# Kernel tuning notes

Measured on AMD Instinct MI355X. Metric: run time of the kernel, lower is better.

Reference implementation:

```python
import jax, jax.numpy as jnp
import numpy as np

NUM_ACTIONS = 16  # number of unique leaf actions (= output_dim)


def setup_inputs() -> dict:
    key = jax.random.key(0)
    ks = jax.random.split(key, 7)
    B, IN, D, A = 32768, 128, 511, 512
    L = D + A + 1  # 1024 leaves
    x = jax.random.normal(ks[0], (B, IN), dtype=jnp.float32)
    Wd = jax.random.normal(ks[1], (D, IN), dtype=jnp.float32) * 0.05
    bd = jax.random.normal(ks[2], (D,), dtype=jnp.float32) * 0.05
    Wa = jax.random.normal(ks[3], (A, IN), dtype=jnp.float32) * 0.05
    ba = jax.random.normal(ks[4], (A,), dtype=jnp.float32) * 0.05
    Wl = jax.random.normal(ks[5], (L, 2 * (D + A)), dtype=jnp.float32) * 0.05
    seg_ids = jax.random.randint(ks[6], (L,), 0, NUM_ACTIONS, dtype=jnp.int32)
    return {"x": x, "Wd": Wd, "bd": bd, "Wa": Wa, "ba": ba, "Wl": Wl,
            "seg_ids": seg_ids}


def reference(x, Wd, bd, Wa, ba, Wl, seg_ids):
    # dual linear heads (torch Linear: y = x @ W.T + b)
    x1 = x @ Wd.T + bd            # [B, D]
    x2 = x @ Wa.T + ba            # [B, A]
    h = jnp.concatenate([x1, x2], axis=1)                     # [B, D+A]
    hh = jnp.concatenate([jax.nn.relu(h), jax.nn.relu(-h)], axis=1)  # [B, 2(D+A)]
    leaf = hh @ Wl.T              # [B, L]
    # ragged per-action max over leaf columns (MaxPoolLayer)
    pooled = jax.ops.segment_max(leaf.T, seg_ids,
                                 num_segments=NUM_ACTIONS).T   # [B, NUM_ACTIONS]
    return jax.nn.softmax(pooled, axis=-1)
```

## Files before the change

kernel.cpp:

```cpp
#include <hip/hip_runtime.h>
#include <hip/hip_bf16.h>
#include <cstdint>
#include <cmath>

#define AS1 __attribute__((address_space(1)))
#define AS3 __attribute__((address_space(3)))

typedef unsigned short u16;
typedef uint32_t u32;
typedef __attribute__((ext_vector_type(8))) __bf16 bf16x8;
typedef __attribute__((ext_vector_type(8))) unsigned short u16x8;
typedef __attribute__((ext_vector_type(4))) float f32x4;


__device__ __forceinline__ u16 f2bf(float f) {
    uint32_t u = __builtin_bit_cast(uint32_t, f);
    return (u16)((u + 0x7fffu + ((u >> 16) & 1u)) >> 16);
}

__device__ __forceinline__ u32 f2ord(float f) {
    u32 u = __builtin_bit_cast(u32, f);
    return u ^ (u32)(((int32_t)u >> 31) | 0x80000000);
}
__device__ __forceinline__ float ord2f(u32 v) {
    u32 u = (v & 0x80000000u) ? (v ^ 0x80000000u) : ~v;
    return __builtin_bit_cast(float, u);
}


__global__ void setup_all(const float* __restrict__ x,
                          const float* __restrict__ Wd, const float* __restrict__ bd,
                          const float* __restrict__ Wa, const float* __restrict__ ba,
                          const float* __restrict__ Wl,
                          u16* __restrict__ xb, u16* __restrict__ w1b,
                          float* __restrict__ bb, u16* __restrict__ w1t,
                          u16* __restrict__ wsb, u16* __restrict__ dlb,
                          float* __restrict__ cl, u32* __restrict__ pooled) {
    __shared__ float cred[256];
    const int b = blockIdx.x;
    const int tid = threadIdx.x;
    if (b < 2048) {
        long idx = (long)(b * 256 + tid) * 8;
        float4 a = *(const float4*)(x + idx);
        float4 c = *(const float4*)(x + idx + 4);
        u16x8 o;
        o[0]=f2bf(a.x); o[1]=f2bf(a.y); o[2]=f2bf(a.z); o[3]=f2bf(a.w);
        o[4]=f2bf(c.x); o[5]=f2bf(c.y); o[6]=f2bf(c.z); o[7]=f2bf(c.w);
        *(u16x8*)(xb + idx) = o;
    } else if (b < 2112) {
        int t = (b - 2048) * 256 + tid;
        int row = t >> 4, g = (t & 15) * 8;
        const float* src = nullptr;
        if (row < 511)       src = Wd + row * 128 + g;
        else if (row < 1023) src = Wa + (row - 511) * 128 + g;
        u16x8 o = 0;
        if (src) {
            #pragma unroll
            for (int j = 0; j < 8; ++j) o[j] = f2bf(src[j]);
        }
        *(u16x8*)(w1b + row * 128 + g) = o;
        #pragma unroll
        for (int j = 0; j < 8; ++j) w1t[(g + j) * 1024 + row] = o[j];
        if ((t & 15) == 0)
            bb[row] = row < 511 ? bd[row] : (row < 1023 ? ba[row - 511] : 0.f);
    } else if (b < 2624) {
        const int l0 = (b - 2112) * 2;
        const int lo = tid >> 7, g = (tid & 127) * 8;
        const float* src = Wl + (long)(l0 + lo) * 2046;
        u16x8 os, od;
        float part = 0.f;
        #pragma unroll
        for (int j = 0; j < 8; ++j) {
            int c = g + j;
            float pa = 0.f, pb = 0.f;
            if (c < 1023) { pa = src[c]; pb = src[1023 + c]; }
            os[j] = f2bf(0.5f * (pa + pb));
            float v = pa - pb;
            od[j] = f2bf(v);
            float b1 = c < 511 ? bd[c] : (c < 1023 ? ba[c - 511] : 0.f);
            part += v * b1;
        }
        *(u16x8*)(wsb + (long)(l0 + lo) * 1024 + g) = os;
        *(u16x8*)(dlb + (long)(l0 + lo) * 1024 + g) = od;
        cred[tid] = part;
        __syncthreads();
        if (tid < 2) {
            float s = 0.f;
            #pragma unroll
            for (int k = 0; k < 128; ++k) s += cred[tid * 128 + k];
            cl[l0 + tid] = 0.5f * s;
        }
    } else {
        uint4* p4 = (uint4*)pooled;
        const int base = (b - 2624) * 16384;
        #pragma unroll
        for (int j = 0; j < 64; ++j)
            p4[base + tid + j * 256] = uint4{0u, 0u, 0u, 0u};
    }
}

__global__ __launch_bounds__(256) void gemm_hwc(
        const u16* __restrict__ xb, const u16* __restrict__ w1b,
        const float* __restrict__ bb,
        const u16* __restrict__ dlb, const u16* __restrict__ w1t,
        u16* __restrict__ habs, u16* __restrict__ wcb) {
    __shared__ union SharedU {
        struct { u16 As[2][4096]; u16 Bs[2][4096]; } s;
        u16 obuf[128 * 132];
    } sh;
    const int tid  = threadIdx.x;
    const int lane = tid & 63, wave = tid >> 6;
    const int wy = wave >> 1, wx = wave & 1;
    const int i16 = lane & 15, q = lane >> 4;
    const int cA = wave * 2, srow = lane >> 2;
    const int scol = (((lane & 3) ^ ((lane >> 3) & 3))) * 8;
    const int qa   = (q ^ ((i16 >> 1) & 3)) * 8;

    f32x4 acc[4][4];
    #pragma unroll
    for (int m = 0; m < 4; ++m)
        #pragma unroll
        for (int n = 0; n < 4; ++n) acc[m][n] = f32x4{0.f,0.f,0.f,0.f};

    if (blockIdx.y == 0) {
        const long blockM = (long)blockIdx.x * 128;
        const int koff = (blockIdx.x * 4) & 31;
        const u16* a0 = dlb + (blockM + cA * 16 + srow) * 1024 + scol;
        const u16* a1 = dlb + (blockM + (cA + 1) * 16 + srow) * 1024 + scol;
        const u16* b0 = w1t + (long)(cA * 16 + srow) * 1024 + scol;
        const u16* b1 = w1t + (long)((cA + 1) * 16 + srow) * 1024 + scol;
        for (int it = 0; it < 32; ++it) {
            const int k0 = ((it + koff) & 31) << 5;
            __builtin_amdgcn_global_load_lds((const AS1 void*)(a0 + k0), (AS3 void*)&sh.s.As[0][cA * 512],       16, 0, 0);
            __builtin_amdgcn_global_load_lds((const AS1 void*)(a1 + k0), (AS3 void*)&sh.s.As[0][(cA + 1) * 512], 16, 0, 0);
            __builtin_amdgcn_global_load_lds((const AS1 void*)(b0 + k0), (AS3 void*)&sh.s.Bs[0][cA * 512],       16, 0, 0);
            __builtin_amdgcn_global_load_lds((const AS1 void*)(b1 + k0), (AS3 void*)&sh.s.Bs[0][(cA + 1) * 512], 16, 0, 0);
            __syncthreads();
            bf16x8 af[4], bfv[4];
            #pragma unroll
            for (int s = 0; s < 4; ++s) {
                af[s]  = *(const bf16x8*)&sh.s.As[0][(wy * 64 + s * 16 + i16) * 32 + qa];
                bfv[s] = *(const bf16x8*)&sh.s.Bs[0][(wx * 64 + s * 16 + i16) * 32 + qa];
            }
            #pragma unroll
            for (int sm = 0; sm < 4; ++sm)
                #pragma unroll
                for (int sn = 0; sn < 4; ++sn)
                    acc[sm][sn] = __builtin_amdgcn_mfma_f32_16x16x32_bf16(af[sm], bfv[sn], acc[sm][sn], 0, 0, 0);
            __syncthreads();
        }
        #pragma unroll
        for (int sm = 0; sm < 4; ++sm)
            #pragma unroll
            for (int sn = 0; sn < 4; ++sn) {
                const int col = wx * 64 + sn * 16 + i16;
                #pragma unroll
                for (int r = 0; r < 4; ++r) {
                    const long row = blockM + wy * 64 + sm * 16 + 4 * q + r;
                    wcb[row * 128 + col] = f2bf(0.5f * acc[sm][sn][r]);
                }
            }
        return;
    }

    const int xcd = blockIdx.x, yy = blockIdx.y - 1;
    const long blockM = (long)(xcd * 32 + (yy >> 3)) * 128;
    const int  blockN = (yy & 7) * 128;
    const int  koff = (yy >> 3) & 1;

    const u16* a0 = xb + (blockM + cA * 16 + srow) * 128 + scol;
    const u16* a1 = xb + (blockM + (cA + 1) * 16 + srow) * 128 + scol;
    const u16* b0 = w1b + ((long)blockN + cA * 16 + srow) * 128 + scol;
    const u16* b1 = w1b + ((long)blockN + (cA + 1) * 16 + srow) * 128 + scol;
    for (int it = 0; it < 2; ++it) {
        const int k0 = ((it + koff) & 1) << 6;
        #pragma unroll
        for (int p = 0; p < 2; ++p) {
            const int kp = k0 + p * 32;
            __builtin_amdgcn_global_load_lds((const AS1 void*)(a0 + kp), (AS3 void*)&sh.s.As[p][cA * 512],       16, 0, 0);
            __builtin_amdgcn_global_load_lds((const AS1 void*)(a1 + kp), (AS3 void*)&sh.s.As[p][(cA + 1) * 512], 16, 0, 0);
            __builtin_amdgcn_global_load_lds((const AS1 void*)(b0 + kp), (AS3 void*)&sh.s.Bs[p][cA * 512],       16, 0, 0);
            __builtin_amdgcn_global_load_lds((const AS1 void*)(b1 + kp), (AS3 void*)&sh.s.Bs[p][(cA + 1) * 512], 16, 0, 0);
        }
        __syncthreads();
        #pragma unroll
        for (int p = 0; p < 2; ++p) {
            bf16x8 af[4], bfv[4];
            #pragma unroll
            for (int s = 0; s < 4; ++s) {
                af[s]  = *(const bf16x8*)&sh.s.As[p][(wy * 64 + s * 16 + i16) * 32 + qa];
                bfv[s] = *(const bf16x8*)&sh.s.Bs[p][(wx * 64 + s * 16 + i16) * 32 + qa];
            }
            #pragma unroll
            for (int sm = 0; sm < 4; ++sm)
                #pragma unroll
                for (int sn = 0; sn < 4; ++sn)
                    acc[sm][sn] = __builtin_amdgcn_mfma_f32_16x16x32_bf16(af[sm], bfv[sn], acc[sm][sn], 0, 0, 0);
        }
        __syncthreads();
    }

    float bv[4];
    #pragma unroll
    for (int sn = 0; sn < 4; ++sn) bv[sn] = bb[blockN + wx * 64 + sn * 16 + i16];
    #pragma unroll
    for (int sm = 0; sm < 4; ++sm)
        #pragma unroll
        for (int sn = 0; sn < 4; ++sn)
            #pragma unroll
            for (int r = 0; r < 4; ++r)
                sh.obuf[(wy * 64 + sm * 16 + 4 * q + r) * 132 + wx * 64 + sn * 16 + i16] =
                    f2bf(fabsf(acc[sm][sn][r] + bv[sn]));
    __syncthreads();
    const int cg = (tid & 15) * 8;
    #pragma unroll
    for (int it = 0; it < 8; ++it) {
        const int row = it * 16 + (tid >> 4);
        *(u16x8*)&habs[(blockM + row) * 1024 + blockN + cg] =
            *(const u16x8*)&sh.obuf[row * 132 + cg];
    }
}

__global__ __launch_bounds__(512, 2) void gemm_leaf(const u16* __restrict__ habs,
        const u16* __restrict__ xb, const u16* __restrict__ wsb,
        const u16* __restrict__ wcb, const float* __restrict__ cl,
        const int* __restrict__ seg, u32* __restrict__ pooled) {
    __shared__ __align__(16) u16 As[4][256 * 32];
    __shared__ __align__(16) u16 Bs[4][256 * 32];
    __shared__ u32 pmax[256 * 16];
    const int tid  = threadIdx.x;
    const int lane = tid & 63, w = tid >> 6;
    const int wm = w >> 2, wn = w & 3;
    const int i16 = lane & 15, q = lane >> 4;

    const int bid  = blockIdx.x;
    const int wgid = (bid & 7) * 64 + (bid >> 3);
    const int mT = wgid >> 2, nT = wgid & 3;
    const long blockM = (long)mT * 256;
    const int  blockN = nT * 256;

    #pragma unroll
    for (int j = 0; j < 8; ++j) pmax[tid + j * 512] = 0u;

    const int r0 = tid >> 2;
    const int scol = (((tid & 3) ^ ((tid >> 3) & 3))) * 8;
    const u16* gA1 = habs + (blockM + r0) * 1024 + scol;
    const u16* gB1 = wsb  + (long)(blockN + r0) * 1024 + scol;
    const u16* gA2 = xb   + (blockM + r0) * 128 + scol;
    const u16* gB2 = wcb  + (long)(blockN + r0) * 128 + scol;
    const int ldsb = w * 512;

    auto stageA = [&](int tt) {
        u16* dst = &As[tt & 3][ldsb];
        const u16* g; int jstr;
        if (tt < 32) { g = gA1 + tt * 32;        jstr = 128 * 1024; }
        else         { g = gA2 + (tt - 32) * 32; jstr = 128 * 128; }
        __builtin_amdgcn_global_load_lds((const AS1 void*)g,          (AS3 void*)dst,          16, 0, 0);
        __builtin_amdgcn_global_load_lds((const AS1 void*)(g + jstr), (AS3 void*)(dst + 4096), 16, 0, 0);
    };
    auto stageB = [&](int tt) {
        u16* dst = &Bs[tt & 3][ldsb];
        const u16* g; int jstr;
        if (tt < 32) { g = gB1 + tt * 32;        jstr = 128 * 1024; }
        else         { g = gB2 + (tt - 32) * 32; jstr = 128 * 128; }
        __builtin_amdgcn_global_load_lds((const AS1 void*)g,          (AS3 void*)dst,          16, 0, 0);
        __builtin_amdgcn_global_load_lds((const AS1 void*)(g + jstr), (AS3 void*)(dst + 4096), 16, 0, 0);
    };

    f32x4 acc[8][4];
    #pragma unroll
    for (int m = 0; m < 8; ++m)
        #pragma unroll
        for (int n = 0; n < 4; ++n) acc[m][n] = f32x4{0.f,0.f,0.f,0.f};
    bf16x8 a0r[4], a1r[4], br[4];

    const int rdc = (q ^ ((i16 >> 1) & 3)) * 8;
    auto lda = [&](bf16x8* ar, int slot, int mh) {
        #pragma unroll
        for (int mf = 0; mf < 4; ++mf)
            ar[mf] = *(const bf16x8*)&As[slot][(wm * 128 + mh * 64 + mf * 16 + i16) * 32 + rdc];
    };
    auto ldb = [&](int slot) {
        #pragma unroll
        for (int nf = 0; nf < 4; ++nf)
            br[nf] = *(const bf16x8*)&Bs[slot][(wn * 64 + nf * 16 + i16) * 32 + rdc];
    };
    auto mf16 = [&](const bf16x8* ar, int mh) {
        #pragma unroll
        for (int mf = 0; mf < 4; ++mf)
            #pragma unroll
            for (int nf = 0; nf < 4; ++nf)
                acc[mh * 4 + mf][nf] = __builtin_amdgcn_mfma_f32_16x16x32_bf16(
                    ar[mf], br[nf], acc[mh * 4 + mf][nf], 0, 0, 0);
    };

    stageA(0); stageB(0); stageA(1); stageB(1);
    asm volatile("s_waitcnt vmcnt(4)" ::: "memory");
    __builtin_amdgcn_s_barrier();
    __builtin_amdgcn_sched_barrier(0);
    lda(a0r, 0, 0); ldb(0);

    for (int t = 0; t < 36; ++t) {
        const int slot = t & 3;
        lda(a1r, slot, 1);
        if (t + 2 < 36) { stageA(t + 2); stageB(t + 2); }
        asm volatile("s_waitcnt lgkmcnt(4)" ::: "memory");
        __builtin_amdgcn_sched_barrier(0);
        __builtin_amdgcn_s_setprio(1);
        mf16(a0r, 0);
        __builtin_amdgcn_s_setprio(0);
        asm volatile("s_waitcnt lgkmcnt(0)" ::: "memory");
        __builtin_amdgcn_sched_barrier(0);
        __builtin_amdgcn_s_setprio(1);
        mf16(a1r, 1);
        __builtin_amdgcn_s_setprio(0);
        if (t < 34)       { asm volatile("s_waitcnt vmcnt(4)" ::: "memory"); }
        else if (t == 34) { asm volatile("s_waitcnt vmcnt(0)" ::: "memory"); }
        __builtin_amdgcn_s_barrier();
        __builtin_amdgcn_sched_barrier(0);
        if (t + 1 < 36) { lda(a0r, (t + 1) & 3, 0); ldb((t + 1) & 3); }
    }

    int segc[4]; float clv[4];
    #pragma unroll
    for (int nf = 0; nf < 4; ++nf) {
        const int col = blockN + wn * 64 + nf * 16 + i16;
        segc[nf] = seg[col];
        clv[nf]  = cl[col];
    }
    #pragma unroll
    for (int mf = 0; mf < 8; ++mf)
        #pragma unroll
        for (int nf = 0; nf < 4; ++nf)
            #pragma unroll
            for (int r = 0; r < 4; ++r) {
                const int rl = wm * 128 + mf * 16 + 4 * q + r;
                atomicMax(&pmax[rl * 16 + segc[nf]], f2ord(acc[mf][nf][r] + clv[nf]));
            }
    __syncthreads();
    #pragma unroll
    for (int j = 0; j < 8; ++j) {
        int idx = tid + j * 512;
        atomicMax(&pooled[((blockM + (idx >> 4)) << 4) + (idx & 15)], pmax[idx]);
    }
}

__global__ __launch_bounds__(256) void finalize(const u32* __restrict__ pooled,
                                                float* __restrict__ out) {
    const int tid = threadIdx.x;
    const long row = (long)blockIdx.x * 16 + (tid >> 4);
    const int t = tid & 15;
    float logit = ord2f(pooled[(row << 4) + t]);
    float rm = logit;
    #pragma unroll
    for (int d = 8; d >= 1; d >>= 1) rm = fmaxf(rm, __shfl_xor(rm, d, 16));
    float e = __expf(logit - rm);
    float s = e;
    #pragma unroll
    for (int d = 8; d >= 1; d >>= 1) s += __shfl_xor(s, d, 16);
    out[(row << 4) + t] = e / s;
}

extern "C" void kernel_launch(void* const* d_in, const int* in_sizes, int n_in,
                              void* d_out, int out_size, void* d_ws, size_t ws_size,
                              hipStream_t stream) {
    const float* x  = (const float*)d_in[0];
    const float* Wd = (const float*)d_in[1];
    const float* bd = (const float*)d_in[2];
    const float* Wa = (const float*)d_in[3];
    const float* ba = (const float*)d_in[4];
    const float* Wl = (const float*)d_in[5];
    const int*  seg = (const int*)d_in[6];
    float* out = (float*)d_out;

    char* ws = (char*)d_ws;
    u16*   xb   = (u16*)(ws);
    u16*   w1b  = (u16*)(ws + 8388608);
    float* bb   = (float*)(ws + 8650752);
    u16*   w1t  = (u16*)(ws + 8654848);
    u16*   wsb  = (u16*)(ws + 8916992);
    u16*   dlb  = (u16*)(ws + 11014144);
    u16*   wcb  = (u16*)(ws + 13111296);
    float* clp  = (float*)(ws + 13373440);
    u16*   habs = (u16*)(ws + 13377536);
    u32*   pooled = (u32*)(ws + 80486400);

    setup_all<<<2632, 256, 0, stream>>>(x, Wd, bd, Wa, ba, Wl,
                                        xb, w1b, bb, w1t, wsb, dlb, clp, pooled);
    gemm_hwc <<<dim3(8, 257), 256, 0, stream>>>(xb, w1b, bb, dlb, w1t, habs, wcb);
    gemm_leaf<<<512, 512, 0, stream>>>(habs, xb, wsb, wcb, clp, seg, pooled);
    finalize <<<2048, 256, 0, stream>>>(pooled, out);
}
```

Baseline: 198.5 us.

## Double-buffer first GEMM k-loop and shrink leaf GEMM LDS ring for occupancy

The first GEMM phase now stages one 32-wide k-slice at a time into a two-slot LDS ring, issuing the next slice's global-to-LDS loads while the MFMAs on the current slice run, instead of loading two slices and then computing with a full barrier in between. The leaf GEMM cuts its LDS ring from four to two slots, prefetches only one step ahead, and raises the launch-bounds occupancy hint from 2 to 4 blocks per CU. The aim is to overlap memory with compute and fit more resident blocks. The cost is a shallower prefetch (waiting on vmcnt(0) every step) and tighter register limits that may cause spills with a 32-tile accumulator.

```diff
diff --git a/kernel.cpp b/kernel.cpp
--- a/kernel.cpp
+++ b/kernel.cpp
@@ -166,38 +166,43 @@
     const int xcd = blockIdx.x, yy = blockIdx.y - 1;
     const long blockM = (long)(xcd * 32 + (yy >> 3)) * 128;
     const int  blockN = (yy & 7) * 128;
-    const int  koff = (yy >> 3) & 1;
 
     const u16* a0 = xb + (blockM + cA * 16 + srow) * 128 + scol;
     const u16* a1 = xb + (blockM + (cA + 1) * 16 + srow) * 128 + scol;
     const u16* b0 = w1b + ((long)blockN + cA * 16 + srow) * 128 + scol;
     const u16* b1 = w1b + ((long)blockN + (cA + 1) * 16 + srow) * 128 + scol;
-    for (int it = 0; it < 2; ++it) {
-        const int k0 = ((it + koff) & 1) << 6;
-        #pragma unroll
-        for (int p = 0; p < 2; ++p) {
-            const int kp = k0 + p * 32;
-            __builtin_amdgcn_global_load_lds((const AS1 void*)(a0 + kp), (AS3 void*)&sh.s.As[p][cA * 512],       16, 0, 0);
-            __builtin_amdgcn_global_load_lds((const AS1 void*)(a1 + kp), (AS3 void*)&sh.s.As[p][(cA + 1) * 512], 16, 0, 0);
-            __builtin_amdgcn_global_load_lds((const AS1 void*)(b0 + kp), (AS3 void*)&sh.s.Bs[p][cA * 512],       16, 0, 0);
-            __builtin_amdgcn_global_load_lds((const AS1 void*)(b1 + kp), (AS3 void*)&sh.s.Bs[p][(cA + 1) * 512], 16, 0, 0);
-        }
-        __syncthreads();
-        #pragma unroll
-        for (int p = 0; p < 2; ++p) {
-            bf16x8 af[4], bfv[4];
-            #pragma unroll
-            for (int s = 0; s < 4; ++s) {
-                af[s]  = *(const bf16x8*)&sh.s.As[p][(wy * 64 + s * 16 + i16) * 32 + qa];
-                bfv[s] = *(const bf16x8*)&sh.s.Bs[p][(wx * 64 + s * 16 + i16) * 32 + qa];
-            }
-            #pragma unroll
-            for (int sm = 0; sm < 4; ++sm)
-                #pragma unroll
-                for (int sn = 0; sn < 4; ++sn)
-                    acc[sm][sn] = __builtin_amdgcn_mfma_f32_16x16x32_bf16(af[sm], bfv[sn], acc[sm][sn], 0, 0, 0);
-        }
-        __syncthreads();
+    auto hstage = [&](int tt) {
+        const int sl = tt & 1, kp = tt * 32;
+        __builtin_amdgcn_global_load_lds((const AS1 void*)(a0 + kp), (AS3 void*)&sh.s.As[sl][cA * 512],       16, 0, 0);
+        __builtin_amdgcn_global_load_lds((const AS1 void*)(a1 + kp), (AS3 void*)&sh.s.As[sl][(cA + 1) * 512], 16, 0, 0);
+        __builtin_amdgcn_global_load_lds((const AS1 void*)(b0 + kp), (AS3 void*)&sh.s.Bs[sl][cA * 512],       16, 0, 0);
+        __builtin_amdgcn_global_load_lds((const AS1 void*)(b1 + kp), (AS3 void*)&sh.s.Bs[sl][(cA + 1) * 512], 16, 0, 0);
+    };
+    hstage(0);
+    asm volatile("s_waitcnt vmcnt(0)" ::: "memory");
+    __builtin_amdgcn_s_barrier();
+    #pragma unroll
+    for (int kt = 0; kt < 4; ++kt) {
+        const int sl = kt & 1;
+        __builtin_amdgcn_sched_barrier(0);
+        bf16x8 af[4], bfv[4];
+        #pragma unroll
+        for (int s = 0; s < 4; ++s) {
+            af[s]  = *(const bf16x8*)&sh.s.As[sl][(wy * 64 + s * 16 + i16) * 32 + qa];
+            bfv[s] = *(const bf16x8*)&sh.s.Bs[sl][(wx * 64 + s * 16 + i16) * 32 + qa];
+        }
+        if (kt + 1 < 4) hstage(kt + 1);
+        asm volatile("s_waitcnt lgkmcnt(0)" ::: "memory");
+        __builtin_amdgcn_sched_barrier(0);
+        __builtin_amdgcn_s_setprio(1);
+        #pragma unroll
+        for (int sm = 0; sm < 4; ++sm)
+            #pragma unroll
+            for (int sn = 0; sn < 4; ++sn)
+                acc[sm][sn] = __builtin_amdgcn_mfma_f32_16x16x32_bf16(af[sm], bfv[sn], acc[sm][sn], 0, 0, 0);
+        __builtin_amdgcn_s_setprio(0);
+        if (kt + 1 < 4) { asm volatile("s_waitcnt vmcnt(0)" ::: "memory"); }
+        __builtin_amdgcn_s_barrier();
     }
 
     float bv[4];
@@ -221,12 +226,12 @@
     }
 }
 
-__global__ __launch_bounds__(512, 2) void gemm_leaf(const u16* __restrict__ habs,
+__global__ __launch_bounds__(512, 4) void gemm_leaf(const u16* __restrict__ habs,
         const u16* __restrict__ xb, const u16* __restrict__ wsb,
         const u16* __restrict__ wcb, const float* __restrict__ cl,
         const int* __restrict__ seg, u32* __restrict__ pooled) {
-    __shared__ __align__(16) u16 As[4][256 * 32];
-    __shared__ __align__(16) u16 Bs[4][256 * 32];
+    __shared__ __align__(16) u16 As[2][256 * 32];
+    __shared__ __align__(16) u16 Bs[2][256 * 32];
     __shared__ u32 pmax[256 * 16];
     const int tid  = threadIdx.x;
     const int lane = tid & 63, w = tid >> 6;
@@ -251,7 +256,7 @@
     const int ldsb = w * 512;
 
     auto stageA = [&](int tt) {
-        u16* dst = &As[tt & 3][ldsb];
+        u16* dst = &As[tt & 1][ldsb];
         const u16* g; int jstr;
         if (tt < 32) { g = gA1 + tt * 32;        jstr = 128 * 1024; }
         else         { g = gA2 + (tt - 32) * 32; jstr = 128 * 128; }
@@ -259,7 +264,7 @@
         __builtin_amdgcn_global_load_lds((const AS1 void*)(g + jstr), (AS3 void*)(dst + 4096), 16, 0, 0);
     };
     auto stageB = [&](int tt) {
-        u16* dst = &Bs[tt & 3][ldsb];
+        u16* dst = &Bs[tt & 1][ldsb];
         const u16* g; int jstr;
         if (tt < 32) { g = gB1 + tt * 32;        jstr = 128 * 1024; }
         else         { g = gB2 + (tt - 32) * 32; jstr = 128 * 128; }
@@ -294,16 +299,16 @@
                     ar[mf], br[nf], acc[mh * 4 + mf][nf], 0, 0, 0);
     };
 
-    stageA(0); stageB(0); stageA(1); stageB(1);
-    asm volatile("s_waitcnt vmcnt(4)" ::: "memory");
+    stageA(0); stageB(0);
+    asm volatile("s_waitcnt vmcnt(0)" ::: "memory");
     __builtin_amdgcn_s_barrier();
     __builtin_amdgcn_sched_barrier(0);
     lda(a0r, 0, 0); ldb(0);
 
     for (int t = 0; t < 36; ++t) {
-        const int slot = t & 3;
+        const int slot = t & 1;
         lda(a1r, slot, 1);
-        if (t + 2 < 36) { stageA(t + 2); stageB(t + 2); }
+        if (t + 1 < 36) { stageA(t + 1); stageB(t + 1); }
         asm volatile("s_waitcnt lgkmcnt(4)" ::: "memory");
         __builtin_amdgcn_sched_barrier(0);
         __builtin_amdgcn_s_setprio(1);
@@ -314,11 +319,10 @@
         __builtin_amdgcn_s_setprio(1);
         mf16(a1r, 1);
         __builtin_amdgcn_s_setprio(0);
-        if (t < 34)       { asm volatile("s_waitcnt vmcnt(4)" ::: "memory"); }
-        else if (t == 34) { asm volatile("s_waitcnt vmcnt(0)" ::: "memory"); }
+        if (t + 1 < 36) { asm volatile("s_waitcnt vmcnt(0)" ::: "memory"); }
         __builtin_amdgcn_s_barrier();
         __builtin_amdgcn_sched_barrier(0);
-        if (t + 1 < 36) { lda(a0r, (t + 1) & 3, 0); ldb((t + 1) & 3); }
+        if (t + 1 < 36) { lda(a0r, (t + 1) & 1, 0); ldb((t + 1) & 1); }
     }
 
     int segc[4]; float clv[4];
```

After: 792.2 us. 3.99x slower.
